# Kernel tuning notes

Hardware: AMD Instinct MI355X
Metric: run time of the kernel (lower is better)

Reference implementation:

```python
import jax, jax.numpy as jnp
import numpy as np

N = 50000      # nodes
E = 640000     # edges (before self loops)
IN = 128       # in_channels
H = 4          # heads (layer 1)
C = 64         # hidden_channels per head
OUT = 64       # out_channels
SLOPE = 0.2    # PyG GATConv default negative_slope


def setup_inputs() -> dict:
    key = jax.random.key(0)
    ks = jax.random.split(key, 12)
    x = jax.random.normal(ks[0], (N, IN), dtype=jnp.float32)
    edge_src = jax.random.randint(ks[1], (E,), 0, N, dtype=jnp.int32)
    edge_dst = jax.random.randint(ks[2], (E,), 0, N, dtype=jnp.int32)
    # Layer 1 params: Linear IN -> H*C, attention vectors a_src/a_dst [H, C], bias [H*C]
    W1 = jax.random.normal(ks[3], (IN, H * C), dtype=jnp.float32) / np.sqrt(IN)
    att_src1 = jax.random.normal(ks[4], (H, C), dtype=jnp.float32) / np.sqrt(C)
    att_dst1 = jax.random.normal(ks[5], (H, C), dtype=jnp.float32) / np.sqrt(C)
    b1 = jnp.zeros((H * C,), dtype=jnp.float32)
    # Layer 2 params: Linear H*C -> OUT, 1 head
    W2 = jax.random.normal(ks[6], (H * C, OUT), dtype=jnp.float32) / np.sqrt(H * C)
    att_src2 = jax.random.normal(ks[7], (1, OUT), dtype=jnp.float32) / np.sqrt(OUT)
    att_dst2 = jax.random.normal(ks[8], (1, OUT), dtype=jnp.float32) / np.sqrt(OUT)
    b2 = jnp.zeros((OUT,), dtype=jnp.float32)
    return {"x": x, "W1": W1, "att_src1": att_src1, "att_dst1": att_dst1, "b1": b1,
            "W2": W2, "att_src2": att_src2, "att_dst2": att_dst2, "b2": b2,
            "edge_src": edge_src, "edge_dst": edge_dst}


def gat_conv(x, src, dst, W, a_src, a_dst, b, heads, ch):
    """PyG GATConv (concat=True): gather -> LeakyReLU attention -> per-dst softmax -> scatter-add."""
    n = x.shape[0]
    h = (x @ W).reshape(n, heads, ch)                  # [N, H, C]
    al_s = jnp.sum(h * a_src, axis=-1)                 # [N, H] node-level src attention term
    al_d = jnp.sum(h * a_dst, axis=-1)                 # [N, H]
    e = jax.nn.leaky_relu(al_s[src] + al_d[dst], SLOPE)  # [E, H] edge scores
    m = jax.ops.segment_max(e, dst, num_segments=n)    # stable per-dst softmax
    ex = jnp.exp(e - m[dst])
    den = jax.ops.segment_sum(ex, dst, num_segments=n)
    alpha = ex / den[dst]                              # [E, H]
    msg = h[src] * alpha[:, :, None]                   # [E, H, C]
    out = jax.ops.segment_sum(msg, dst, num_segments=n)  # [N, H, C]
    return out.reshape(n, heads * ch) + b


def reference(x, W1, att_src1, att_dst1, b1, W2, att_src2, att_dst2, b2, edge_src, edge_dst):
    # PyG GATConv default add_self_loops=True
    loops = jnp.arange(N, dtype=edge_src.dtype)
    src = jnp.concatenate([edge_src, loops])
    dst = jnp.concatenate([edge_dst, loops])
    h = gat_conv(x, src, dst, W1, att_src1, att_dst1, b1, H, C)
    h = jax.nn.elu(h)                                  # F.elu; dropout p=0 -> no-op
    out = gat_conv(h, src, dst, W2, att_src2, att_dst2, b2, 1, OUT)
    return out
```

## Files before the change

### kernel.cpp

```cpp
#include <hip/hip_runtime.h>
#include <hip/hip_bf16.h>
#include <cstdint>
#include <cstddef>

#define N_NODES 50000
#define N_EDGES 640000
#define ET (N_EDGES + N_NODES)
#define IN_CH 128
#define H1 4
#define HC1 256
#define OUT_CH 64
#define SLOPE 0.2f
#define SCAN_NBLK ((N_NODES + 255) / 256)
#define XW (N_NODES * IN_CH / 8)
#define W1N (IN_CH * HC1)
#define W2N (HC1 * OUT_CH)
#define CONVB ((XW + W1N + W2N + 255) / 256)
#define EDGEB ((ET + 255) / 256)
#define MT ((N_NODES + 63) / 64)
#define G1B (4 * MT)

typedef __attribute__((ext_vector_type(8))) short short8;
typedef __attribute__((ext_vector_type(4))) float floatx4;

__device__ __forceinline__ float bf2f(unsigned short u) {
    return __uint_as_float(((unsigned)u) << 16);
}
__device__ __forceinline__ unsigned short f2bf(float f) {
    unsigned u = __float_as_uint(f);
    unsigned r = 0x7fffu + ((u >> 16) & 1u);
    return (unsigned short)((u + r) >> 16);
}
__device__ __forceinline__ float ldf(const void* p, size_t i, bool f32) {
    return f32 ? ((const float*)p)[i] : bf2f(((const unsigned short*)p)[i]);
}
#define BLO(u) __uint_as_float((u) << 16)
#define BHI(u) __uint_as_float((u) & 0xffff0000u)

__global__ __launch_bounds__(256) void init_all(
    const unsigned short* __restrict__ x, unsigned* __restrict__ flag,
    int* __restrict__ counts, int* __restrict__ state)
{
    int b = blockIdx.x;
    if (b < SCAN_NBLK) {
        int i = b * 256 + threadIdx.x;
        if (i < N_NODES) counts[i] = 0;
    } else {
        int t = threadIdx.x;
        if (t < 64) {
            int bad = 0;
            #pragma unroll
            for (int r = 0; r < 4; ++r) {
                float v = bf2f(x[r * 64 + t]);
                if (!(v == v) || fabsf(v) > 1e4f) bad = 1;
            }
            unsigned long long m = __ballot(bad != 0);
            if (t == 0) *flag = (m != 0ull) ? 1u : 0u;
        } else if (t == 64) {
            state[0] = 0; state[1] = 0;
        }
    }
}

__global__ __launch_bounds__(256) void conv_count(
    const void* __restrict__ x, const void* __restrict__ W1,
    const void* __restrict__ W2, const unsigned* __restrict__ flag,
    unsigned short* __restrict__ x16,
    unsigned short* __restrict__ Wt1, unsigned short* __restrict__ Wt2,
    const int* __restrict__ edst, int* __restrict__ counts,
    int* __restrict__ epos)
{
    int b = blockIdx.x;
    if (b < CONVB) {
        int i = b * 256 + threadIdx.x;
        const bool f32 = (*flag != 0);
        if (i < XW) {
            size_t off = (size_t)i * 8;
            uint4 st;
            if (f32) {
                const float* xp = (const float*)x + off;
                float4 a = *(const float4*)xp;
                float4 c = *(const float4*)(xp + 4);
                st.x = (unsigned)f2bf(a.x) | ((unsigned)f2bf(a.y) << 16);
                st.y = (unsigned)f2bf(a.z) | ((unsigned)f2bf(a.w) << 16);
                st.z = (unsigned)f2bf(c.x) | ((unsigned)f2bf(c.y) << 16);
                st.w = (unsigned)f2bf(c.z) | ((unsigned)f2bf(c.w) << 16);
            } else {
                st = *(const uint4*)((const unsigned short*)x + off);
            }
            *(uint4*)(x16 + off) = st;
        } else if (i < XW + W1N) {
            int j = i - XW;
            int n = j / IN_CH, k = j % IN_CH;
            Wt1[j] = f2bf(ldf(W1, (size_t)k * HC1 + n, f32));
        } else if (i < XW + W1N + W2N) {
            int j = i - XW - W1N;
            int n = j / HC1, k = j % HC1;
            Wt2[j] = f2bf(ldf(W2, (size_t)k * OUT_CH + n, f32));
        }
    } else {
        int i = (b - CONVB) * 256 + threadIdx.x;
        if (i < ET) {
            int d = (i < N_EDGES) ? edst[i] : (i - N_EDGES);
            epos[i] = atomicAdd(&counts[d], 1);
        }
    }
}

__global__ __launch_bounds__(256) void scan_onepass(
    const int* __restrict__ counts, int* __restrict__ rowptr,
    int* __restrict__ bsum, int* __restrict__ boff, int* __restrict__ state)
{
    __shared__ int s[256];
    const int t = threadIdx.x, b = blockIdx.x;
    const int i = b * 256 + t;
    int v = (i < N_NODES) ? counts[i] : 0;
    s[t] = v;
    __syncthreads();
    #pragma unroll
    for (int off = 1; off < 256; off <<= 1) {
        int u = (t >= off) ? s[t - off] : 0;
        __syncthreads();
        s[t] += u;
        __syncthreads();
    }
    const int incl = s[t];
    if (t == 255) {
        __hip_atomic_store(&bsum[b], incl, __ATOMIC_RELAXED, __HIP_MEMORY_SCOPE_AGENT);
        __hip_atomic_fetch_add(&state[0], 1, __ATOMIC_ACQ_REL, __HIP_MEMORY_SCOPE_AGENT);
    }
    if (b == 0) {
        if (t == 0) {
            while (__hip_atomic_load(&state[0], __ATOMIC_ACQUIRE, __HIP_MEMORY_SCOPE_AGENT) < SCAN_NBLK)
                __builtin_amdgcn_s_sleep(8);
        }
        __syncthreads();
        int w = (t < SCAN_NBLK)
              ? __hip_atomic_load(&bsum[t], __ATOMIC_RELAXED, __HIP_MEMORY_SCOPE_AGENT) : 0;
        s[t] = w;
        __syncthreads();
        #pragma unroll
        for (int off = 1; off < 256; off <<= 1) {
            int u = (t >= off) ? s[t - off] : 0;
            __syncthreads();
            s[t] += u;
            __syncthreads();
        }
        if (t < SCAN_NBLK)
            __hip_atomic_store(&boff[t], s[t] - w, __ATOMIC_RELAXED, __HIP_MEMORY_SCOPE_AGENT);
        __syncthreads();
        if (t == 0)
            __hip_atomic_store(&state[1], 1, __ATOMIC_RELEASE, __HIP_MEMORY_SCOPE_AGENT);
    }
    if (t == 0) {
        while (__hip_atomic_load(&state[1], __ATOMIC_ACQUIRE, __HIP_MEMORY_SCOPE_AGENT) == 0)
            __builtin_amdgcn_s_sleep(8);
    }
    __syncthreads();
    int off0 = __hip_atomic_load(&boff[b], __ATOMIC_RELAXED, __HIP_MEMORY_SCOPE_AGENT);
    if (i < N_NODES)
        rowptr[i] = off0 + incl - v;
    if (i == N_NODES - 1) rowptr[N_NODES] = off0 + incl;
}

template <int KK, int NSUB>
__device__ __forceinline__ void gemm_body(
    const unsigned short* __restrict__ A, const unsigned short* __restrict__ Bt,
    const void* __restrict__ avs, const void* __restrict__ avd,
    const unsigned* __restrict__ flag, unsigned short* __restrict__ C,
    float* __restrict__ als, float* __restrict__ ald,
    int M, int N, int bx, int by)
{
    const int tid = threadIdx.x;
    const int m0 = by * 64, n0 = bx * (NSUB * 16);
    const int w = tid >> 6, lane = tid & 63;
    const int ln = lane & 15, quad = lane >> 4;
    const int m_frag = m0 + w * 16 + ln;
    floatx4 acc[NSUB];
    #pragma unroll
    for (int sub = 0; sub < NSUB; ++sub)
        acc[sub] = (floatx4){0.f, 0.f, 0.f, 0.f};

    for (int ks = 0; ks < KK / 32; ++ks) {
        const int kbase = ks * 32 + quad * 8;
        short8 a;
        if (m_frag < M) {
            a = *(const short8*)(A + (size_t)m_frag * KK + kbase);
        } else {
            #pragma unroll
            for (int j = 0; j < 8; ++j) a[j] = 0;
        }
        #pragma unroll
        for (int sub = 0; sub < NSUB; ++sub) {
            short8 b = *(const short8*)(Bt + (size_t)(n0 + sub * 16 + ln) * KK + kbase);
            acc[sub] = __builtin_amdgcn_mfma_f32_16x16x32_bf16(a, b, acc[sub], 0, 0, 0);
        }
    }

    #pragma unroll
    for (int sub = 0; sub < NSUB; ++sub) {
        #pragma unroll
        for (int r = 0; r < 4; ++r) {
            int m = m0 + w * 16 + quad * 4 + r;
            if (m < M)
                C[(size_t)m * N + n0 + sub * 16 + ln] = f2bf(acc[sub][r]);
        }
    }

    const bool f32in = (*flag != 0);
    float as[NSUB], av[NSUB];
    #pragma unroll
    for (int sub = 0; sub < NSUB; ++sub) {
        as[sub] = ldf(avs, n0 + sub * 16 + ln, f32in);
        av[sub] = ldf(avd, n0 + sub * 16 + ln, f32in);
    }
    const int Hh = N >> 6;
    #pragma unroll
    for (int hb = 0; hb < NSUB / 4; ++hb) {
        #pragma unroll
        for (int r = 0; r < 4; ++r) {
            float ps = 0.f, pd = 0.f;
            #pragma unroll
            for (int k = 0; k < 4; ++k) {
                ps += acc[hb * 4 + k][r] * as[hb * 4 + k];
                pd += acc[hb * 4 + k][r] * av[hb * 4 + k];
            }
            #pragma unroll
            for (int off = 1; off < 16; off <<= 1) {
                ps += __shfl_xor(ps, off, 64);
                pd += __shfl_xor(pd, off, 64);
            }
            int m = m0 + w * 16 + quad * 4 + r;
            if (ln == 0 && m < M) {
                als[(size_t)m * Hh + bx * (NSUB / 4) + hb] = ps;
                ald[(size_t)m * Hh + bx * (NSUB / 4) + hb] = pd;
            }
        }
    }
}

__global__ __launch_bounds__(256) void gemm1_fill(
    const unsigned short* __restrict__ x16, const unsigned short* __restrict__ Wt1,
    const void* __restrict__ as1, const void* __restrict__ ad1,
    const unsigned* __restrict__ flag, unsigned short* __restrict__ h16,
    float* __restrict__ als, float* __restrict__ ald,
    const int* __restrict__ esrc, const int* __restrict__ edst,
    const int* __restrict__ rowptr, const int* __restrict__ epos,
    int* __restrict__ ecsr)
{
    int b = blockIdx.x;
    if (b < G1B) {
        gemm_body<IN_CH, 4>(x16, Wt1, as1, ad1, flag, h16, als, ald,
                            N_NODES, HC1, b & 3, b >> 2);
    } else {
        int i = (b - G1B) * 256 + threadIdx.x;
        if (i < ET) {
            int s = (i < N_EDGES) ? esrc[i] : (i - N_EDGES);
            int d = (i < N_EDGES) ? edst[i] : (i - N_EDGES);
            ecsr[rowptr[d] + epos[i]] = s;
        }
    }
}

__global__ __launch_bounds__(256) void edge_w1(
    const int* __restrict__ esrc, const int* __restrict__ edst,
    const int* __restrict__ rowptr, const int* __restrict__ epos,
    const float* __restrict__ als1, const float* __restrict__ ald1,
    float* __restrict__ ew1)
{
    int i = blockIdx.x * 256 + threadIdx.x;
    if (i >= ET) return;
    int s = (i < N_EDGES) ? esrc[i] : (i - N_EDGES);
    int d = (i < N_EDGES) ? edst[i] : (i - N_EDGES);
    int slot = rowptr[d] + epos[i];
    float4 as = *(const float4*)(als1 + (size_t)s * H1);
    float4 ad = *(const float4*)(ald1 + (size_t)d * H1);
    float t0 = as.x + ad.x, t1 = as.y + ad.y;
    float t2 = as.z + ad.z, t3 = as.w + ad.w;
    ew1[0 * (size_t)ET + slot] = __expf(fmaxf(t0, SLOPE * t0));
    ew1[1 * (size_t)ET + slot] = __expf(fmaxf(t1, SLOPE * t1));
    ew1[2 * (size_t)ET + slot] = __expf(fmaxf(t2, SLOPE * t2));
    ew1[3 * (size_t)ET + slot] = __expf(fmaxf(t3, SLOPE * t3));
}

__global__ __launch_bounds__(256) void agg_node1(
    const int* __restrict__ rowptr, const int* __restrict__ ecsr,
    const unsigned short* __restrict__ h, const float* __restrict__ ew1,
    const void* __restrict__ bias, const unsigned* __restrict__ flag,
    unsigned short* __restrict__ out)
{
    int wave = (blockIdx.x * blockDim.x + threadIdx.x) >> 6;
    int lane = threadIdx.x & 63;
    if (wave >= N_NODES) return;
    const int d = wave;
    const int hg = lane >> 4;
    const int c0 = (lane & 15) << 2;
    const int hoff = hg * 64 + c0;
    const int lo = rowptr[d], hi = rowptr[d + 1];
    const float* __restrict__ ewh = ew1 + (size_t)hg * ET;

    float acc0 = 0.f, acc1 = 0.f, acc2 = 0.f, acc3 = 0.f, den = 0.f;

    int e = lo;
    for (; e + 3 < hi; e += 4) {
        int s0 = ecsr[e], s1 = ecsr[e + 1], s2 = ecsr[e + 2], s3 = ecsr[e + 3];
        float p0 = ewh[e], p1 = ewh[e + 1], p2 = ewh[e + 2], p3 = ewh[e + 3];
        uint2 q0 = *(const uint2*)(h + (size_t)s0 * HC1 + hoff);
        uint2 q1 = *(const uint2*)(h + (size_t)s1 * HC1 + hoff);
        uint2 q2 = *(const uint2*)(h + (size_t)s2 * HC1 + hoff);
        uint2 q3 = *(const uint2*)(h + (size_t)s3 * HC1 + hoff);
        den += (p0 + p1) + (p2 + p3);
        acc0 += p0 * BLO(q0.x) + p1 * BLO(q1.x) + p2 * BLO(q2.x) + p3 * BLO(q3.x);
        acc1 += p0 * BHI(q0.x) + p1 * BHI(q1.x) + p2 * BHI(q2.x) + p3 * BHI(q3.x);
        acc2 += p0 * BLO(q0.y) + p1 * BLO(q1.y) + p2 * BLO(q2.y) + p3 * BLO(q3.y);
        acc3 += p0 * BHI(q0.y) + p1 * BHI(q1.y) + p2 * BHI(q2.y) + p3 * BHI(q3.y);
    }
    for (; e < hi; ++e) {
        int s0 = ecsr[e];
        float p0 = ewh[e];
        uint2 q0 = *(const uint2*)(h + (size_t)s0 * HC1 + hoff);
        den += p0;
        acc0 += p0 * BLO(q0.x);
        acc1 += p0 * BHI(q0.x);
        acc2 += p0 * BLO(q0.y);
        acc3 += p0 * BHI(q0.y);
    }

    const bool f32in = (*flag != 0);
    const float inv = 1.f / den;
    float v0 = acc0 * inv + ldf(bias, hoff + 0, f32in);
    float v1 = acc1 * inv + ldf(bias, hoff + 1, f32in);
    float v2 = acc2 * inv + ldf(bias, hoff + 2, f32in);
    float v3 = acc3 * inv + ldf(bias, hoff + 3, f32in);
    v0 = (v0 > 0.f) ? v0 : (__expf(v0) - 1.f);
    v1 = (v1 > 0.f) ? v1 : (__expf(v1) - 1.f);
    v2 = (v2 > 0.f) ? v2 : (__expf(v2) - 1.f);
    v3 = (v3 > 0.f) ? v3 : (__expf(v3) - 1.f);
    uint2 st;
    st.x = (unsigned)f2bf(v0) | ((unsigned)f2bf(v1) << 16);
    st.y = (unsigned)f2bf(v2) | ((unsigned)f2bf(v3) << 16);
    *(uint2*)(out + (size_t)d * HC1 + hoff) = st;
}

__global__ __launch_bounds__(256) void gemm2(
    const unsigned short* __restrict__ xo16, const unsigned short* __restrict__ Wt2,
    const void* __restrict__ as2, const void* __restrict__ ad2,
    const unsigned* __restrict__ flag, unsigned short* __restrict__ h2,
    float* __restrict__ als, float* __restrict__ ald)
{
    gemm_body<HC1, 4>(xo16, Wt2, as2, ad2, flag, h2, als, ald,
                      N_NODES, OUT_CH, 0, blockIdx.x);
}

__global__ __launch_bounds__(256) void agg_node2(
    const int* __restrict__ rowptr, const int* __restrict__ ecsr,
    const unsigned short* __restrict__ h, const float* __restrict__ als,
    const float* __restrict__ ald, const void* __restrict__ bias,
    const unsigned* __restrict__ flag, float* __restrict__ out)
{
    int wave = (blockIdx.x * blockDim.x + threadIdx.x) >> 6;
    int lane = threadIdx.x & 63;
    if (wave >= N_NODES) return;
    const int d = wave;
    const int eg = lane >> 3;
    const int c0 = (lane & 7) << 3;
    const int lo = rowptr[d], hi = rowptr[d + 1];
    const float ad = ald[d];

    float acc[8];
    #pragma unroll
    for (int j = 0; j < 8; ++j) acc[j] = 0.f;
    float den = 0.f;

    for (int eb = lo; eb < hi; eb += 8) {
        int e = eb + eg;
        if (e < hi) {
            int s = ecsr[e];
            uint4 q = *(const uint4*)(h + (size_t)s * OUT_CH + c0);
            float t = als[s] + ad;
            float p = __expf(fmaxf(t, SLOPE * t));
            den += p;
            acc[0] += p * BLO(q.x);
            acc[1] += p * BHI(q.x);
            acc[2] += p * BLO(q.y);
            acc[3] += p * BHI(q.y);
            acc[4] += p * BLO(q.z);
            acc[5] += p * BHI(q.z);
            acc[6] += p * BLO(q.w);
            acc[7] += p * BHI(q.w);
        }
    }
    #pragma unroll
    for (int off = 8; off <= 32; off <<= 1) {
        den += __shfl_xor(den, off, 64);
        #pragma unroll
        for (int j = 0; j < 8; ++j) acc[j] += __shfl_xor(acc[j], off, 64);
    }
    if (lane < 8) {
        const bool f32in = (*flag != 0);
        const float inv = 1.f / den;
        float4 v0, v1;
        v0.x = acc[0] * inv + ldf(bias, c0 + 0, f32in);
        v0.y = acc[1] * inv + ldf(bias, c0 + 1, f32in);
        v0.z = acc[2] * inv + ldf(bias, c0 + 2, f32in);
        v0.w = acc[3] * inv + ldf(bias, c0 + 3, f32in);
        v1.x = acc[4] * inv + ldf(bias, c0 + 4, f32in);
        v1.y = acc[5] * inv + ldf(bias, c0 + 5, f32in);
        v1.z = acc[6] * inv + ldf(bias, c0 + 6, f32in);
        v1.w = acc[7] * inv + ldf(bias, c0 + 7, f32in);
        *(float4*)(out + (size_t)d * OUT_CH + c0) = v0;
        *(float4*)(out + (size_t)d * OUT_CH + c0 + 4) = v1;
    }
}

extern "C" void kernel_launch(void* const* d_in, const int* in_sizes, int n_in,
                              void* d_out, int out_size, void* d_ws, size_t ws_size,
                              hipStream_t stream)
{
    const void* x   = d_in[0];
    const void* W1  = d_in[1];
    const void* as1 = d_in[2];
    const void* ad1 = d_in[3];
    const void* b1  = d_in[4];
    const void* W2  = d_in[5];
    const void* as2 = d_in[6];
    const void* ad2 = d_in[7];
    const void* b2  = d_in[8];
    const int* esrc = (const int*)d_in[9];
    const int* edst = (const int*)d_in[10];
    float* out = (float*)d_out;

    char* base = (char*)d_ws;
    const size_t MB = 1024 * 1024;
    unsigned short* x16  = (unsigned short*)(base);
    float* ew1           = (float*)(base);
    unsigned short* h16  = (unsigned short*)(base + 13 * MB);
    unsigned short* xo16 = (unsigned short*)(base + 39 * MB);
    unsigned short* h2   = (unsigned short*)(base + 65 * MB);
    float* als1   = (float*)(base + 72 * MB);
    float* ald1   = (float*)(base + 73 * MB);
    float* als2   = (float*)(base + 74 * MB);
    float* ald2   = (float*)(base + 74 * MB + 512 * 1024);
    unsigned short* Wt1 = (unsigned short*)(base + 75 * MB);
    unsigned short* Wt2 = (unsigned short*)(base + 75 * MB + 128 * 1024);
    int* counts   = (int*)(base + 76 * MB);
    int* rowptr   = (int*)(base + 77 * MB);
    int* bsum     = (int*)(base + 78 * MB);
    int* boff     = bsum + 256;
    int* state    = boff + 256;
    unsigned* flag = (unsigned*)(base + 78 * MB + 8 * 1024);
    int* epos     = (int*)(base + 79 * MB);
    int* ecsr     = (int*)(base + 82 * MB);

    const int BLK = 256;
    const int node_wave_blocks = (N_NODES * 64 + BLK - 1) / BLK;

    init_all<<<SCAN_NBLK + 1, BLK, 0, stream>>>(
        (const unsigned short*)x, flag, counts, state);

    conv_count<<<CONVB + EDGEB, BLK, 0, stream>>>(
        x, W1, W2, flag, x16, Wt1, Wt2, edst, counts, epos);

    scan_onepass<<<SCAN_NBLK, BLK, 0, stream>>>(
        counts, rowptr, bsum, boff, state);

    gemm1_fill<<<G1B + EDGEB, BLK, 0, stream>>>(
        x16, Wt1, as1, ad1, flag, h16, als1, ald1, esrc, edst, rowptr, epos,
        ecsr);

    edge_w1<<<EDGEB, BLK, 0, stream>>>(
        esrc, edst, rowptr, epos, als1, ald1, ew1);

    agg_node1<<<node_wave_blocks, BLK, 0, stream>>>(
        rowptr, ecsr, h16, ew1, b1, flag, xo16);

    gemm2<<<MT, BLK, 0, stream>>>(xo16, Wt2, as2, ad2, flag, h2, als2, ald2);

    agg_node2<<<node_wave_blocks, BLK, 0, stream>>>(
        rowptr, ecsr, h2, als2, ald2, b2, flag, out);
}
```

Measured before the change: 323.2 us.

## Fuse scan into GEMM1/fill kernel, compute edge weights inline, drop init kernel

Replaces the init kernel with a memset and moves the x-dtype probe into the conversion kernel. The separate scan kernel is folded into the GEMM1/CSR-fill launch: fill blocks spin on a completion counter until the scan blocks are done. The edge_w1 pass and its edge-weight buffer are removed; agg_node1 now computes the leaky-relu exp weights on the fly from per-node attention terms. GEMM1 tiles are widened to 8 subtiles, halving the block count. This cuts three launches and one global pass over edges, in exchange for redundant exp work per head, extra gathers, and a spin-wait dependency that relies on scan blocks being scheduled before fill blocks.

Result: faster. 296.8 us (-8.2%).

```diff
diff --git a/kernel.cpp b/kernel.cpp
--- a/kernel.cpp
+++ b/kernel.cpp
@@ -18,7 +18,7 @@
 #define CONVB ((XW + W1N + W2N + 255) / 256)
 #define EDGEB ((ET + 255) / 256)
 #define MT ((N_NODES + 63) / 64)
-#define G1B (4 * MT)
+#define G1B (2 * MT)
 
 typedef __attribute__((ext_vector_type(8))) short short8;
 typedef __attribute__((ext_vector_type(4))) float floatx4;
@@ -37,34 +37,21 @@
 #define BLO(u) __uint_as_float((u) << 16)
 #define BHI(u) __uint_as_float((u) & 0xffff0000u)
 
-__global__ __launch_bounds__(256) void init_all(
-    const unsigned short* __restrict__ x, unsigned* __restrict__ flag,
-    int* __restrict__ counts, int* __restrict__ state)
-{
-    int b = blockIdx.x;
-    if (b < SCAN_NBLK) {
-        int i = b * 256 + threadIdx.x;
-        if (i < N_NODES) counts[i] = 0;
-    } else {
-        int t = threadIdx.x;
-        if (t < 64) {
-            int bad = 0;
-            #pragma unroll
-            for (int r = 0; r < 4; ++r) {
-                float v = bf2f(x[r * 64 + t]);
-                if (!(v == v) || fabsf(v) > 1e4f) bad = 1;
-            }
-            unsigned long long m = __ballot(bad != 0);
-            if (t == 0) *flag = (m != 0ull) ? 1u : 0u;
-        } else if (t == 64) {
-            state[0] = 0; state[1] = 0;
-        }
-    }
+__device__ __forceinline__ bool probe_f32(const unsigned short* x) {
+    int t = threadIdx.x & 63;
+    int bad = 0;
+    #pragma unroll
+    for (int r = 0; r < 4; ++r) {
+        float v = bf2f(x[r * 64 + t]);
+        if (!(v == v) || fabsf(v) > 1e4f) bad = 1;
+    }
+    unsigned long long m = __ballot(bad != 0);
+    return m != 0ull;
 }
 
 __global__ __launch_bounds__(256) void conv_count(
     const void* __restrict__ x, const void* __restrict__ W1,
-    const void* __restrict__ W2, const unsigned* __restrict__ flag,
+    const void* __restrict__ W2, unsigned* __restrict__ flag,
     unsigned short* __restrict__ x16,
     unsigned short* __restrict__ Wt1, unsigned short* __restrict__ Wt2,
     const int* __restrict__ edst, int* __restrict__ counts,
@@ -72,8 +59,9 @@
 {
     int b = blockIdx.x;
     if (b < CONVB) {
+        const bool f32 = probe_f32((const unsigned short*)x);
+        if (b == 0 && threadIdx.x == 0) *flag = f32 ? 1u : 0u;
         int i = b * 256 + threadIdx.x;
-        const bool f32 = (*flag != 0);
         if (i < XW) {
             size_t off = (size_t)i * 8;
             uint4 st;
@@ -107,62 +95,6 @@
     }
 }
 
-__global__ __launch_bounds__(256) void scan_onepass(
-    const int* __restrict__ counts, int* __restrict__ rowptr,
-    int* __restrict__ bsum, int* __restrict__ boff, int* __restrict__ state)
-{
-    __shared__ int s[256];
-    const int t = threadIdx.x, b = blockIdx.x;
-    const int i = b * 256 + t;
-    int v = (i < N_NODES) ? counts[i] : 0;
-    s[t] = v;
-    __syncthreads();
-    #pragma unroll
-    for (int off = 1; off < 256; off <<= 1) {
-        int u = (t >= off) ? s[t - off] : 0;
-        __syncthreads();
-        s[t] += u;
-        __syncthreads();
-    }
-    const int incl = s[t];
-    if (t == 255) {
-        __hip_atomic_store(&bsum[b], incl, __ATOMIC_RELAXED, __HIP_MEMORY_SCOPE_AGENT);
-        __hip_atomic_fetch_add(&state[0], 1, __ATOMIC_ACQ_REL, __HIP_MEMORY_SCOPE_AGENT);
-    }
-    if (b == 0) {
-        if (t == 0) {
-            while (__hip_atomic_load(&state[0], __ATOMIC_ACQUIRE, __HIP_MEMORY_SCOPE_AGENT) < SCAN_NBLK)
-                __builtin_amdgcn_s_sleep(8);
-        }
-        __syncthreads();
-        int w = (t < SCAN_NBLK)
-              ? __hip_atomic_load(&bsum[t], __ATOMIC_RELAXED, __HIP_MEMORY_SCOPE_AGENT) : 0;
-        s[t] = w;
-        __syncthreads();
-        #pragma unroll
-        for (int off = 1; off < 256; off <<= 1) {
-            int u = (t >= off) ? s[t - off] : 0;
-            __syncthreads();
-            s[t] += u;
-            __syncthreads();
-        }
-        if (t < SCAN_NBLK)
-            __hip_atomic_store(&boff[t], s[t] - w, __ATOMIC_RELAXED, __HIP_MEMORY_SCOPE_AGENT);
-        __syncthreads();
-        if (t == 0)
-            __hip_atomic_store(&state[1], 1, __ATOMIC_RELEASE, __HIP_MEMORY_SCOPE_AGENT);
-    }
-    if (t == 0) {
-        while (__hip_atomic_load(&state[1], __ATOMIC_ACQUIRE, __HIP_MEMORY_SCOPE_AGENT) == 0)
-            __builtin_amdgcn_s_sleep(8);
-    }
-    __syncthreads();
-    int off0 = __hip_atomic_load(&boff[b], __ATOMIC_RELAXED, __HIP_MEMORY_SCOPE_AGENT);
-    if (i < N_NODES)
-        rowptr[i] = off0 + incl - v;
-    if (i == N_NODES - 1) rowptr[N_NODES] = off0 + incl;
-}
-
 template <int KK, int NSUB>
 __device__ __forceinline__ void gemm_body(
     const unsigned short* __restrict__ A, const unsigned short* __restrict__ Bt,
@@ -239,55 +171,99 @@
     }
 }
 
-__global__ __launch_bounds__(256) void gemm1_fill(
+__global__ __launch_bounds__(256) void gemm1_scan_fill(
+    const int* __restrict__ counts, int* __restrict__ rowptr,
+    int* __restrict__ bsum, int* __restrict__ boff, int* __restrict__ state,
     const unsigned short* __restrict__ x16, const unsigned short* __restrict__ Wt1,
     const void* __restrict__ as1, const void* __restrict__ ad1,
     const unsigned* __restrict__ flag, unsigned short* __restrict__ h16,
     float* __restrict__ als, float* __restrict__ ald,
     const int* __restrict__ esrc, const int* __restrict__ edst,
-    const int* __restrict__ rowptr, const int* __restrict__ epos,
-    int* __restrict__ ecsr)
-{
-    int b = blockIdx.x;
-    if (b < G1B) {
-        gemm_body<IN_CH, 4>(x16, Wt1, as1, ad1, flag, h16, als, ald,
-                            N_NODES, HC1, b & 3, b >> 2);
+    const int* __restrict__ epos, int* __restrict__ ecsr)
+{
+    const int b = blockIdx.x;
+    const int t = threadIdx.x;
+    if (b < SCAN_NBLK) {
+        __shared__ int s[256];
+        const int i = b * 256 + t;
+        int v = (i < N_NODES) ? counts[i] : 0;
+        s[t] = v;
+        __syncthreads();
+        #pragma unroll
+        for (int off = 1; off < 256; off <<= 1) {
+            int u = (t >= off) ? s[t - off] : 0;
+            __syncthreads();
+            s[t] += u;
+            __syncthreads();
+        }
+        const int incl = s[t];
+        if (t == 255) {
+            __hip_atomic_store(&bsum[b], incl, __ATOMIC_RELAXED, __HIP_MEMORY_SCOPE_AGENT);
+            __hip_atomic_fetch_add(&state[0], 1, __ATOMIC_ACQ_REL, __HIP_MEMORY_SCOPE_AGENT);
+        }
+        if (b == 0) {
+            if (t == 0) {
+                while (__hip_atomic_load(&state[0], __ATOMIC_ACQUIRE, __HIP_MEMORY_SCOPE_AGENT) < SCAN_NBLK)
+                    __builtin_amdgcn_s_sleep(8);
+            }
+            __syncthreads();
+            int w = (t < SCAN_NBLK)
+                  ? __hip_atomic_load(&bsum[t], __ATOMIC_RELAXED, __HIP_MEMORY_SCOPE_AGENT) : 0;
+            s[t] = w;
+            __syncthreads();
+            #pragma unroll
+            for (int off = 1; off < 256; off <<= 1) {
+                int u = (t >= off) ? s[t - off] : 0;
+                __syncthreads();
+                s[t] += u;
+                __syncthreads();
+            }
+            if (t < SCAN_NBLK)
+                __hip_atomic_store(&boff[t], s[t] - w, __ATOMIC_RELAXED, __HIP_MEMORY_SCOPE_AGENT);
+            __syncthreads();
+            if (t == 0)
+                __hip_atomic_store(&state[1], 1, __ATOMIC_RELEASE, __HIP_MEMORY_SCOPE_AGENT);
+        }
+        if (t == 0) {
+            while (__hip_atomic_load(&state[1], __ATOMIC_ACQUIRE, __HIP_MEMORY_SCOPE_AGENT) == 0)
+                __builtin_amdgcn_s_sleep(8);
+        }
+        __syncthreads();
+        int off0 = __hip_atomic_load(&boff[b], __ATOMIC_RELAXED, __HIP_MEMORY_SCOPE_AGENT);
+        if (i < N_NODES)
+            __hip_atomic_store(&rowptr[i], off0 + incl - v,
+                               __ATOMIC_RELAXED, __HIP_MEMORY_SCOPE_AGENT);
+        if (i == N_NODES - 1)
+            __hip_atomic_store(&rowptr[N_NODES], off0 + incl,
+                               __ATOMIC_RELAXED, __HIP_MEMORY_SCOPE_AGENT);
+        __syncthreads();
+        if (t == 0)
+            __hip_atomic_fetch_add(&state[2], 1, __ATOMIC_ACQ_REL, __HIP_MEMORY_SCOPE_AGENT);
+    } else if (b < SCAN_NBLK + G1B) {
+        int g = b - SCAN_NBLK;
+        gemm_body<IN_CH, 8>(x16, Wt1, as1, ad1, flag, h16, als, ald,
+                            N_NODES, HC1, g & 1, g >> 1);
     } else {
-        int i = (b - G1B) * 256 + threadIdx.x;
+        if (t == 0) {
+            while (__hip_atomic_load(&state[2], __ATOMIC_ACQUIRE, __HIP_MEMORY_SCOPE_AGENT) < SCAN_NBLK)
+                __builtin_amdgcn_s_sleep(8);
+        }
+        __syncthreads();
+        int i = (b - SCAN_NBLK - G1B) * 256 + t;
         if (i < ET) {
             int s = (i < N_EDGES) ? esrc[i] : (i - N_EDGES);
             int d = (i < N_EDGES) ? edst[i] : (i - N_EDGES);
-            ecsr[rowptr[d] + epos[i]] = s;
-        }
-    }
-}
-
-__global__ __launch_bounds__(256) void edge_w1(
-    const int* __restrict__ esrc, const int* __restrict__ edst,
-    const int* __restrict__ rowptr, const int* __restrict__ epos,
-    const float* __restrict__ als1, const float* __restrict__ ald1,
-    float* __restrict__ ew1)
-{
-    int i = blockIdx.x * 256 + threadIdx.x;
-    if (i >= ET) return;
-    int s = (i < N_EDGES) ? esrc[i] : (i - N_EDGES);
-    int d = (i < N_EDGES) ? edst[i] : (i - N_EDGES);
-    int slot = rowptr[d] + epos[i];
-    float4 as = *(const float4*)(als1 + (size_t)s * H1);
-    float4 ad = *(const float4*)(ald1 + (size_t)d * H1);
-    float t0 = as.x + ad.x, t1 = as.y + ad.y;
-    float t2 = as.z + ad.z, t3 = as.w + ad.w;
-    ew1[0 * (size_t)ET + slot] = __expf(fmaxf(t0, SLOPE * t0));
-    ew1[1 * (size_t)ET + slot] = __expf(fmaxf(t1, SLOPE * t1));
-    ew1[2 * (size_t)ET + slot] = __expf(fmaxf(t2, SLOPE * t2));
-    ew1[3 * (size_t)ET + slot] = __expf(fmaxf(t3, SLOPE * t3));
+            int rp = __hip_atomic_load(&rowptr[d], __ATOMIC_RELAXED, __HIP_MEMORY_SCOPE_AGENT);
+            ecsr[rp + epos[i]] = s;
+        }
+    }
 }
 
 __global__ __launch_bounds__(256) void agg_node1(
     const int* __restrict__ rowptr, const int* __restrict__ ecsr,
-    const unsigned short* __restrict__ h, const float* __restrict__ ew1,
-    const void* __restrict__ bias, const unsigned* __restrict__ flag,
-    unsigned short* __restrict__ out)
+    const unsigned short* __restrict__ h, const float* __restrict__ als,
+    const float* __restrict__ ald, const void* __restrict__ bias,
+    const unsigned* __restrict__ flag, unsigned short* __restrict__ out)
 {
     int wave = (blockIdx.x * blockDim.x + threadIdx.x) >> 6;
     int lane = threadIdx.x & 63;
@@ -297,33 +273,30 @@
     const int c0 = (lane & 15) << 2;
     const int hoff = hg * 64 + c0;
     const int lo = rowptr[d], hi = rowptr[d + 1];
-    const float* __restrict__ ewh = ew1 + (size_t)hg * ET;
+    const float ad = ald[d * H1 + hg];
 
     float acc0 = 0.f, acc1 = 0.f, acc2 = 0.f, acc3 = 0.f, den = 0.f;
 
-    int e = lo;
-    for (; e + 3 < hi; e += 4) {
-        int s0 = ecsr[e], s1 = ecsr[e + 1], s2 = ecsr[e + 2], s3 = ecsr[e + 3];
-        float p0 = ewh[e], p1 = ewh[e + 1], p2 = ewh[e + 2], p3 = ewh[e + 3];
+    for (int e = lo; e < hi; e += 4) {
+        int e1 = min(e + 1, hi - 1), e2 = min(e + 2, hi - 1), e3 = min(e + 3, hi - 1);
+        int s0 = ecsr[e],  s1 = ecsr[e1], s2 = ecsr[e2], s3 = ecsr[e3];
+        float t0 = als[s0 * H1 + hg] + ad;
+        float t1 = als[s1 * H1 + hg] + ad;
+        float t2 = als[s2 * H1 + hg] + ad;
+        float t3 = als[s3 * H1 + hg] + ad;
         uint2 q0 = *(const uint2*)(h + (size_t)s0 * HC1 + hoff);
         uint2 q1 = *(const uint2*)(h + (size_t)s1 * HC1 + hoff);
         uint2 q2 = *(const uint2*)(h + (size_t)s2 * HC1 + hoff);
         uint2 q3 = *(const uint2*)(h + (size_t)s3 * HC1 + hoff);
+        float p0 = __expf(fmaxf(t0, SLOPE * t0));
+        float p1 = (e + 1 < hi) ? __expf(fmaxf(t1, SLOPE * t1)) : 0.f;
+        float p2 = (e + 2 < hi) ? __expf(fmaxf(t2, SLOPE * t2)) : 0.f;
+        float p3 = (e + 3 < hi) ? __expf(fmaxf(t3, SLOPE * t3)) : 0.f;
         den += (p0 + p1) + (p2 + p3);
         acc0 += p0 * BLO(q0.x) + p1 * BLO(q1.x) + p2 * BLO(q2.x) + p3 * BLO(q3.x);
         acc1 += p0 * BHI(q0.x) + p1 * BHI(q1.x) + p2 * BHI(q2.x) + p3 * BHI(q3.x);
         acc2 += p0 * BLO(q0.y) + p1 * BLO(q1.y) + p2 * BLO(q2.y) + p3 * BLO(q3.y);
         acc3 += p0 * BHI(q0.y) + p1 * BHI(q1.y) + p2 * BHI(q2.y) + p3 * BHI(q3.y);
-    }
-    for (; e < hi; ++e) {
-        int s0 = ecsr[e];
-        float p0 = ewh[e];
-        uint2 q0 = *(const uint2*)(h + (size_t)s0 * HC1 + hoff);
-        den += p0;
-        acc0 += p0 * BLO(q0.x);
-        acc1 += p0 * BHI(q0.x);
-        acc2 += p0 * BLO(q0.y);
-        acc3 += p0 * BHI(q0.y);
     }
 
     const bool f32in = (*flag != 0);
@@ -433,7 +406,6 @@
     char* base = (char*)d_ws;
     const size_t MB = 1024 * 1024;
     unsigned short* x16  = (unsigned short*)(base);
-    float* ew1           = (float*)(base);
     unsigned short* h16  = (unsigned short*)(base + 13 * MB);
     unsigned short* xo16 = (unsigned short*)(base + 39 * MB);
     unsigned short* h2   = (unsigned short*)(base + 65 * MB);
@@ -444,10 +416,10 @@
     unsigned short* Wt1 = (unsigned short*)(base + 75 * MB);
     unsigned short* Wt2 = (unsigned short*)(base + 75 * MB + 128 * 1024);
     int* counts   = (int*)(base + 76 * MB);
+    int* state    = counts + N_NODES;
     int* rowptr   = (int*)(base + 77 * MB);
     int* bsum     = (int*)(base + 78 * MB);
     int* boff     = bsum + 256;
-    int* state    = boff + 256;
     unsigned* flag = (unsigned*)(base + 78 * MB + 8 * 1024);
     int* epos     = (int*)(base + 79 * MB);
     int* ecsr     = (int*)(base + 82 * MB);
@@ -455,24 +427,17 @@
     const int BLK = 256;
     const int node_wave_blocks = (N_NODES * 64 + BLK - 1) / BLK;
 
-    init_all<<<SCAN_NBLK + 1, BLK, 0, stream>>>(
-        (const unsigned short*)x, flag, counts, state);
+    hipMemsetAsync(counts, 0, (size_t)N_NODES * 4 + 12, stream);
 
     conv_count<<<CONVB + EDGEB, BLK, 0, stream>>>(
         x, W1, W2, flag, x16, Wt1, Wt2, edst, counts, epos);
 
-    scan_onepass<<<SCAN_NBLK, BLK, 0, stream>>>(
-        counts, rowptr, bsum, boff, state);
-
-    gemm1_fill<<<G1B + EDGEB, BLK, 0, stream>>>(
-        x16, Wt1, as1, ad1, flag, h16, als1, ald1, esrc, edst, rowptr, epos,
-        ecsr);
-
-    edge_w1<<<EDGEB, BLK, 0, stream>>>(
-        esrc, edst, rowptr, epos, als1, ald1, ew1);
+    gemm1_scan_fill<<<SCAN_NBLK + G1B + EDGEB, BLK, 0, stream>>>(
+        counts, rowptr, bsum, boff, state, x16, Wt1, as1, ad1, flag,
+        h16, als1, ald1, esrc, edst, epos, ecsr);
 
     agg_node1<<<node_wave_blocks, BLK, 0, stream>>>(
-        rowptr, ecsr, h16, ew1, b1, flag, xo16);
+        rowptr, ecsr, h16, als1, ald1, b1, flag, xo16);
 
     gemm2<<<MT, BLK, 0, stream>>>(xo16, Wt2, as2, ad2, flag, h2, als2, ald2);
 
```
